# Optimization experiments

Hardware: AMD Instinct MI355X
Metric: run time of the kernel (lower is better)

Reference implementation:

```python
import jax, jax.numpy as jnp
import numpy as np

B, C, L = 4, 64, 4096
RED = 4          # reduction -> q/k channels = C // RED = 16
N_HASHES = 4
HASH_BUCKETS = min(L // 4, 32)  # = 32, matches torch code
EPS = 1e-5


def _conv1x1(x, W, b):
    # x: [B, Cin, L], W: [Cout, Cin], b: [Cout]
    return jnp.einsum('bcl,oc->bol', x, W) + b[None, :, None]


def setup_inputs() -> dict:
    key = jax.random.key(0)
    ks = jax.random.split(key, 12)
    Cq = C // RED
    x = jax.random.normal(ks[0], (B, C, L), dtype=jnp.float32)
    hash_idx = jax.random.randint(ks[1], (B, N_HASHES, L), 0, HASH_BUCKETS, dtype=jnp.int32)
    sC = 1.0 / np.sqrt(C)
    Wq = jax.random.normal(ks[2], (Cq, C), dtype=jnp.float32) * sC
    bq = jax.random.normal(ks[3], (Cq,), dtype=jnp.float32) * 0.01
    Wk = jax.random.normal(ks[4], (Cq, C), dtype=jnp.float32) * sC
    bk = jax.random.normal(ks[5], (Cq,), dtype=jnp.float32) * 0.01
    Wv = jax.random.normal(ks[6], (C, C), dtype=jnp.float32) * sC
    bv = jax.random.normal(ks[7], (C,), dtype=jnp.float32) * 0.01
    Wo = jax.random.normal(ks[8], (C, C), dtype=jnp.float32) * sC
    bo = jax.random.normal(ks[9], (C,), dtype=jnp.float32) * 0.01
    gamma = jax.random.normal(ks[10], (1,), dtype=jnp.float32)  # nonzero so attn path matters
    bn_w = jnp.ones((C,), dtype=jnp.float32)
    bn_b = jnp.zeros((C,), dtype=jnp.float32)
    return dict(x=x, hash_idx=hash_idx, Wq=Wq, bq=bq, Wk=Wk, bk=bk,
                Wv=Wv, bv=bv, Wo=Wo, bo=bo, gamma=gamma, bn_w=bn_w, bn_b=bn_b)


def reference(x, hash_idx, Wq, bq, Wk, bk, Wv, bv, Wo, bo, gamma, bn_w, bn_b):
    # 1x1 conv projections
    q = _conv1x1(x, Wq, bq)   # [B, C/RED, L]
    k = _conv1x1(x, Wk, bk)   # [B, C/RED, L]
    v = _conv1x1(x, Wv, bv)   # [B, C, L]

    qT = q.transpose(0, 2, 1)  # [B, L, Cq]
    kT = k.transpose(0, 2, 1)
    vT = v.transpose(0, 2, 1)  # [B, L, C]

    # raw scores are hash-independent; only the bucket mask changes per hash
    scores = jnp.einsum('bic,bjc->bij', qT, kT)  # [B, L, L], no sqrt(d) scaling (matches torch)

    n_hashes = hash_idx.shape[1]
    acc = jnp.zeros_like(vT)
    for h in range(n_hashes):  # small fixed loop
        idx = hash_idx[:, h, :]                       # [B, L]
        mask = idx[:, :, None] == idx[:, None, :]     # same-bucket mask [B, L, L]
        s = jnp.where(mask, scores, -1e9)
        attn = jax.nn.softmax(s, axis=-1)             # within-bucket softmax (diag always valid)
        acc = acc + jnp.einsum('bij,bjc->bic', attn, vT)
    attn_out = (acc / n_hashes).transpose(0, 2, 1)    # [B, C, L], averaged over hashes

    out = _conv1x1(attn_out, Wo, bo)
    out = gamma * out + x                             # residual with learned scalar

    # BatchNorm1d, training mode: biased batch stats over (B, L) per channel
    mean = out.mean(axis=(0, 2), keepdims=True)
    var = out.var(axis=(0, 2), keepdims=True)
    out = (out - mean) * jax.lax.rsqrt(var + EPS)
    out = out * bn_w[None, :, None] + bn_b[None, :, None]
    return out
```

## Files before the change

kernel.cpp:

```cpp
#include <hip/hip_runtime.h>
#include <math.h>

#define Bn 4
#define Cn 64
#define Ln 4096
#define CQ 16
#define NH 4
#define NB 32
#define EPSV 1e-5f

#define MAXS 384
#define CH2 64
#define KSTR 20
#define VSTR 64

#define QSZ   (Bn*Ln*CQ)
#define VSZ   (Bn*Ln*Cn)
#define ACCSZ (Bn*Ln*Cn)
#define NBH   (Bn*NH)

#define OFF_K   QSZ
#define OFF_V   (2*QSZ)
#define OFF_ACC (2*QSZ + VSZ)

#define LOG2E 1.44269504088896f

__global__ __launch_bounds__(256) void proj_kernel(
        const float* __restrict__ x,
        const float* __restrict__ Wq, const float* __restrict__ bq,
        const float* __restrict__ Wk, const float* __restrict__ bk,
        const float* __restrict__ Wv, const float* __restrict__ bv,
        float* __restrict__ q, float* __restrict__ k, float* __restrict__ v) {
    __shared__ float sWt[Cn*32];
    __shared__ float sb[32];
    int tid = threadIdx.x;
    int third = blockIdx.x % 3;
    int pg    = blockIdx.x / 3;
    int rbase = third * 32;
    for (int idx = tid; idx < Cn*32; idx += 256) {
        int rr = idx & 31, c = idx >> 5;
        int r = rbase + rr;
        float w;
        if (r < 16)      w = Wq[r*Cn + c];
        else if (r < 32) w = Wk[(r-16)*Cn + c];
        else             w = Wv[(r-32)*Cn + c];
        sWt[c*32 + rr] = w;
    }
    if (tid < 32) {
        int r = rbase + tid;
        sb[tid] = (r < 16) ? bq[r] : (r < 32 ? bk[r-16] : bv[r-32]);
    }
    __syncthreads();
    int p = tid & 63, og = tid >> 6;
    int gp = pg * 64 + p;
    int b = gp >> 12, l = gp & (Ln - 1);
    const float* xp = &x[b*Cn*Ln + l];
    int rr0 = og * 8;
    float val[8];
    #pragma unroll
    for (int i = 0; i < 8; i++) val[i] = sb[rr0 + i];
    #pragma unroll
    for (int c0 = 0; c0 < Cn; c0 += 8) {
        float xv[8];
        #pragma unroll
        for (int i = 0; i < 8; i++) xv[i] = xp[(c0 + i)*Ln];
        #pragma unroll
        for (int i = 0; i < 8; i++) {
            const float* wrow = &sWt[(c0 + i)*32 + rr0];
            #pragma unroll
            for (int j = 0; j < 8; j++) val[j] = fmaf(wrow[j], xv[i], val[j]);
        }
    }
    int f = third*8 + og*2;
    float4 t0 = make_float4(val[0], val[1], val[2], val[3]);
    float4 t1 = make_float4(val[4], val[5], val[6], val[7]);
    float4* q4 = (float4*)&q[gp*CQ];
    float4* k4 = (float4*)&k[gp*CQ];
    float4* v4 = (float4*)&v[gp*Cn];
    if (f < 4)      { q4[f]   = t0; q4[f+1] = t1; }
    else if (f < 8) { k4[f-4] = t0; k4[f-3] = t1; }
    else            { v4[f-8] = t0; v4[f-7] = t1; }
}

template<int NS, int MODE>
__device__ __forceinline__ void attn_pass(
        int qbase, int S, int b, int h, int tid,
        const int* list, float* ks, float* vs,
        const float* __restrict__ q, const float* __restrict__ k,
        const float* __restrict__ v, float* __restrict__ acc) {
    int qd = tid >> 2, c4 = tid & 3;
    float4 qr[NS][4];
    float4 o[NS][4];
    float lsum[NS];
    int qi[NS], iqr[NS];
    #pragma unroll
    for (int s = 0; s < NS; s++) {
        qi[s] = qbase + 128*s + qd;
        iqr[s] = 0;
        lsum[s] = 0.f;
        #pragma unroll
        for (int i = 0; i < 4; i++) o[s][i] = make_float4(0.f,0.f,0.f,0.f);
        if (qi[s] < S) {
            iqr[s] = list[qi[s]];
            const float4* qp = (const float4*)&q[(b*Ln + iqr[s])*CQ];
            #pragma unroll
            for (int i = 0; i < 4; i++) {
                float4 t = qp[i];
                t.x*=LOG2E; t.y*=LOG2E; t.z*=LOG2E; t.w*=LOG2E;
                qr[s][i] = t;
            }
        } else {
            #pragma unroll
            for (int i = 0; i < 4; i++) qr[s][i] = make_float4(0.f,0.f,0.f,0.f);
        }
    }
    for (int cc = 0; cc < S; cc += CH2) {
        int nk = min(CH2, S - cc);
        __syncthreads();
        {
            int jj = tid >> 2, cf = tid & 3;
            if (jj < nk) {
                const float4* kp = (const float4*)&k[(b*Ln + list[cc+jj])*CQ];
                *(float4*)&ks[jj*KSTR + cf*4] = kp[cf];
            }
        }
        #pragma unroll
        for (int uu = 0; uu < 2; uu++) {
            int idx = uu*512 + tid;
            int jj = idx >> 4, cf = idx & 15;
            if (jj < nk) {
                const float4* vp = (const float4*)&v[(b*Ln + list[cc+jj])*Cn];
                *(float4*)&vs[jj*VSTR + cf*4] = vp[cf];
            }
        }
        __syncthreads();
        for (int j = 0; j < nk; j++) {
            const float4* kr = (const float4*)&ks[j*KSTR];
            float4 k0 = kr[0], k1 = kr[1], k2 = kr[2], k3 = kr[3];
            const float4* vp4 = (const float4*)&vs[j*VSTR + c4*16];
            float4 v0 = vp4[0], v1 = vp4[1], v2 = vp4[2], v3 = vp4[3];
            #pragma unroll
            for (int s = 0; s < NS; s++) {
                float s0 = qr[s][0].x*k0.x + qr[s][0].y*k0.y + qr[s][0].z*k0.z + qr[s][0].w*k0.w;
                float s1 = qr[s][1].x*k1.x + qr[s][1].y*k1.y + qr[s][1].z*k1.z + qr[s][1].w*k1.w;
                float s2 = qr[s][2].x*k2.x + qr[s][2].y*k2.y + qr[s][2].z*k2.z + qr[s][2].w*k2.w;
                float s3 = qr[s][3].x*k3.x + qr[s][3].y*k3.y + qr[s][3].z*k3.z + qr[s][3].w*k3.w;
                float pw = __builtin_amdgcn_exp2f((s0 + s1) + (s2 + s3));
                lsum[s] += pw;
                o[s][0].x = fmaf(pw, v0.x, o[s][0].x); o[s][0].y = fmaf(pw, v0.y, o[s][0].y);
                o[s][0].z = fmaf(pw, v0.z, o[s][0].z); o[s][0].w = fmaf(pw, v0.w, o[s][0].w);
                o[s][1].x = fmaf(pw, v1.x, o[s][1].x); o[s][1].y = fmaf(pw, v1.y, o[s][1].y);
                o[s][1].z = fmaf(pw, v1.z, o[s][1].z); o[s][1].w = fmaf(pw, v1.w, o[s][1].w);
                o[s][2].x = fmaf(pw, v2.x, o[s][2].x); o[s][2].y = fmaf(pw, v2.y, o[s][2].y);
                o[s][2].z = fmaf(pw, v2.z, o[s][2].z); o[s][2].w = fmaf(pw, v2.w, o[s][2].w);
                o[s][3].x = fmaf(pw, v3.x, o[s][3].x); o[s][3].y = fmaf(pw, v3.y, o[s][3].y);
                o[s][3].z = fmaf(pw, v3.z, o[s][3].z); o[s][3].w = fmaf(pw, v3.w, o[s][3].w);
            }
        }
    }
    #pragma unroll
    for (int s = 0; s < NS; s++) {
        if (qi[s] < S) {
            float inv = 1.f / lsum[s];
            #pragma unroll
            for (int i = 0; i < 4; i++) {
                o[s][i].x*=inv; o[s][i].y*=inv; o[s][i].z*=inv; o[s][i].w*=inv;
            }
            if (MODE == 1) {
                float4* ap = (float4*)&acc[((size_t)h*Bn*Ln + b*Ln + iqr[s])*Cn + c4*16];
                ap[0]=o[s][0]; ap[1]=o[s][1]; ap[2]=o[s][2]; ap[3]=o[s][3];
            } else {
                float* ap = &acc[(b*Ln + iqr[s])*Cn + c4*16];
                #pragma unroll
                for (int i = 0; i < 4; i++) {
                    atomicAdd(&ap[4*i+0], (&o[s][i].x)[0]);
                    atomicAdd(&ap[4*i+1], (&o[s][i].x)[1]);
                    atomicAdd(&ap[4*i+2], (&o[s][i].x)[2]);
                    atomicAdd(&ap[4*i+3], (&o[s][i].x)[3]);
                }
            }
        }
    }
}

template<int MODE>
__global__ __launch_bounds__(512, 4) void attn_kernel(
        const float* __restrict__ q, const float* __restrict__ k,
        const float* __restrict__ v, const int* __restrict__ hidx,
        float* __restrict__ acc) {
    __shared__ int list[MAXS];
    __shared__ float ks[CH2*KSTR];
    __shared__ float vs[CH2*VSTR];
    __shared__ int wtot[8];
    int blk = blockIdx.x;
    int u  = blk & (NB-1);
    int bh = blk >> 5;
    int b  = bh >> 2;
    int h  = bh & 3;
    int tid = threadIdx.x;

    const int4* hp4 = (const int4*)(&hidx[bh*Ln] + tid*8);
    int hv[8];
    {
        int4 t0 = hp4[0], t1 = hp4[1];
        hv[0]=t0.x; hv[1]=t0.y; hv[2]=t0.z; hv[3]=t0.w;
        hv[4]=t1.x; hv[5]=t1.y; hv[6]=t1.z; hv[7]=t1.w;
    }
    int myCnt = 0;
    #pragma unroll
    for (int t = 0; t < 8; t++) myCnt += (hv[t] == u);
    int lane = tid & 63, wv = tid >> 6;
    int pre = myCnt;
    #pragma unroll
    for (int d = 1; d < 64; d <<= 1) {
        int t = __shfl_up(pre, d, 64);
        if (lane >= d) pre += t;
    }
    if (lane == 63) wtot[wv] = pre;
    __syncthreads();
    int base = 0, Sall = 0;
    #pragma unroll
    for (int w = 0; w < 8; w++) {
        base += (w < wv) ? wtot[w] : 0;
        Sall += wtot[w];
    }
    int S = min(Sall, MAXS);
    int excl = base + pre - myCnt;
    #pragma unroll
    for (int t = 0; t < 8; t++) {
        if (hv[t] == u) {
            if (excl < MAXS) list[excl] = tid*8 + t;
            excl++;
        }
    }
    __syncthreads();

    int wq0 = wv * 16;
    for (int qbase = 0; qbase < S; qbase += 256) {
        int rem = S - qbase - wq0;
        if (rem > 128) attn_pass<2,MODE>(qbase,S,b,h,tid,list,ks,vs,q,k,v,acc);
        else           attn_pass<1,MODE>(qbase,S,b,h,tid,list,ks,vs,q,k,v,acc);
    }
}

template<int MODE>
__global__ __launch_bounds__(256) void outconv_kernel(
        const float* __restrict__ acc, const float* __restrict__ Wo,
        const float* __restrict__ bo, const float* __restrict__ gamma,
        const float* __restrict__ x, float* __restrict__ y) {
    __shared__ float sWt[Cn*32];
    __shared__ float sb[32];
    int tid = threadIdx.x;
    int half = blockIdx.x & 1;
    int pg   = blockIdx.x >> 1;
    for (int idx = tid; idx < Cn*32; idx += 256) {
        int oo = idx & 31, c = idx >> 5;
        sWt[c*32 + oo] = Wo[(half*32 + oo)*Cn + c];
    }
    if (tid < 32) sb[tid] = bo[half*32 + tid];
    __syncthreads();
    float g = gamma[0];
    int p = tid & 63, og = tid >> 6;
    int gp = pg * 64 + p;
    int b = gp >> 12, l = gp & (Ln - 1);
    int oo0 = og * 8;
    float val[8];
    #pragma unroll
    for (int i = 0; i < 8; i++) val[i] = sb[oo0 + i];
    const float4* ap0 = (const float4*)&acc[(size_t)gp*Cn];
    #pragma unroll
    for (int c4 = 0; c4 < 16; c4++) {
        float4 t = ap0[c4];
        if (MODE == 1) {
            float4 t1 = ap0[(size_t)ACCSZ/4   + c4];
            float4 t2 = ap0[(size_t)ACCSZ/4*2 + c4];
            float4 t3 = ap0[(size_t)ACCSZ/4*3 + c4];
            t.x += t1.x + t2.x + t3.x; t.y += t1.y + t2.y + t3.y;
            t.z += t1.z + t2.z + t3.z; t.w += t1.w + t2.w + t3.w;
        }
        float a0 = t.x*0.25f, a1 = t.y*0.25f, a2 = t.z*0.25f, a3 = t.w*0.25f;
        const float* w0 = &sWt[(c4*4+0)*32 + oo0];
        const float* w1 = &sWt[(c4*4+1)*32 + oo0];
        const float* w2 = &sWt[(c4*4+2)*32 + oo0];
        const float* w3 = &sWt[(c4*4+3)*32 + oo0];
        #pragma unroll
        for (int i = 0; i < 8; i++) {
            val[i] = fmaf(w0[i], a0, val[i]);
            val[i] = fmaf(w1[i], a1, val[i]);
            val[i] = fmaf(w2[i], a2, val[i]);
            val[i] = fmaf(w3[i], a3, val[i]);
        }
    }
    #pragma unroll
    for (int i = 0; i < 8; i++) {
        int o = half*32 + oo0 + i;
        float yv = fmaf(g, val[i], x[(b*Cn + o)*Ln + l]);
        y[(b*Cn + o)*Ln + l] = yv;
    }
}

__global__ __launch_bounds__(256) void stats_kernel(
        const float* __restrict__ y, float* __restrict__ ssum, float* __restrict__ ssq) {
    int c = blockIdx.x >> 2;
    int part = blockIdx.x & 3;
    int tid = threadIdx.x;
    const float4* yp = (const float4*)&y[(part*Cn + c)*Ln];
    float s = 0.f, s2 = 0.f;
    #pragma unroll
    for (int i = 0; i < 4; i++) {
        float4 t = yp[i*256 + tid];
        s  += t.x + t.y + t.z + t.w;
        s2 += t.x*t.x + t.y*t.y + t.z*t.z + t.w*t.w;
    }
    #pragma unroll
    for (int w = 1; w < 64; w <<= 1) {
        s  += __shfl_xor(s,  w, 64);
        s2 += __shfl_xor(s2, w, 64);
    }
    __shared__ float rs[4], rs2[4];
    int wv = tid >> 6;
    if ((tid & 63) == 0) { rs[wv] = s; rs2[wv] = s2; }
    __syncthreads();
    if (tid == 0) {
        atomicAdd(&ssum[c], rs[0]+rs[1]+rs[2]+rs[3]);
        atomicAdd(&ssq[c],  rs2[0]+rs2[1]+rs2[2]+rs2[3]);
    }
}

__global__ __launch_bounds__(256) void norm_kernel(
        const float* __restrict__ y,
        const float* __restrict__ ssum, const float* __restrict__ ssq,
        const float* __restrict__ bnw, const float* __restrict__ bnb,
        float* __restrict__ out) {
    int idx = blockIdx.x * 256 + threadIdx.x;
    int flat = idx * 4;
    int c = (flat / Ln) & 63;
    const float n = (float)(Bn*Ln);
    float mu = ssum[c] / n;
    float var = ssq[c] / n - mu*mu;
    float is = rsqrtf(var + EPSV);
    float w = is * bnw[c];
    float bb = bnb[c] - mu * w;
    float4 t = ((const float4*)y)[idx];
    float4 r;
    r.x = t.x*w + bb; r.y = t.y*w + bb; r.z = t.z*w + bb; r.w = t.w*w + bb;
    ((float4*)out)[idx] = r;
}

extern "C" void kernel_launch(void* const* d_in, const int* in_sizes, int n_in,
                              void* d_out, int out_size, void* d_ws, size_t ws_size,
                              hipStream_t stream) {
    const float* x    = (const float*)d_in[0];
    const int*   hidx = (const int*)  d_in[1];
    const float* Wq   = (const float*)d_in[2];
    const float* bq   = (const float*)d_in[3];
    const float* Wk   = (const float*)d_in[4];
    const float* bk   = (const float*)d_in[5];
    const float* Wv   = (const float*)d_in[6];
    const float* bv   = (const float*)d_in[7];
    const float* Wo   = (const float*)d_in[8];
    const float* bo   = (const float*)d_in[9];
    const float* gam  = (const float*)d_in[10];
    const float* bnw  = (const float*)d_in[11];
    const float* bnb  = (const float*)d_in[12];
    float* out = (float*)d_out;

    float* ws  = (float*)d_ws;
    float* q   = ws;
    float* k   = ws + OFF_K;
    float* v   = ws + OFF_V;
    float* acc = ws + OFF_ACC;
    float* y   = ws;

    const size_t bigNeed = ((size_t)OFF_ACC + 4*(size_t)ACCSZ + 2*Cn) * sizeof(float);
    bool big = ws_size >= bigNeed;
    float* ssum = acc + (big ? 4*(size_t)ACCSZ : (size_t)ACCSZ);
    float* ssq  = ssum + Cn;

    hipMemsetAsync(ssum, 0, 2*Cn*sizeof(float), stream);

    proj_kernel<<<Bn*Ln/64*3, 256, 0, stream>>>(x, Wq, bq, Wk, bk, Wv, bv, q, k, v);
    if (big) {
        attn_kernel<1><<<NBH*NB, 512, 0, stream>>>(q, k, v, hidx, acc);
        outconv_kernel<1><<<Bn*Ln/64*2, 256, 0, stream>>>(acc, Wo, bo, gam, x, y);
    } else {
        hipMemsetAsync(acc, 0, (size_t)ACCSZ*sizeof(float), stream);
        attn_kernel<0><<<NBH*NB, 512, 0, stream>>>(q, k, v, hidx, acc);
        outconv_kernel<0><<<Bn*Ln/64*2, 256, 0, stream>>>(acc, Wo, bo, gam, x, y);
    }
    stats_kernel<<<Cn*4, 256, 0, stream>>>(y, ssum, ssq);
    norm_kernel<<<Bn*Cn*Ln/4/256, 256, 0, stream>>>(y, ssum, ssq, bnw, bnb, out);
}
```

Measured before the change: 187.2 us.

## Split attention key loop across two block halves and drop stats memset

The attention block now splits its 8 waves into two halves that each process half of a 128-key chunk for the same 64-query tile. The partial outputs and softmax sums are merged through shared memory before normalization. The goal is to halve the query tile per pass so that small buckets keep more waves busy and the loop has less serial length per thread. In exchange it adds extra barriers, a shared-memory reduction step and a larger K/V staging tile. Separately, the BN stats kernel writes per-block partial sums that the norm kernel adds up, which removes the memset and the atomics.

Result: slower. 200.2 us (+7.0%).

```diff
diff --git a/kernel.cpp b/kernel.cpp
--- a/kernel.cpp
+++ b/kernel.cpp
@@ -10,7 +10,7 @@
 #define EPSV 1e-5f
 
 #define MAXS 384
-#define CH2 64
+#define CH2 128
 #define KSTR 20
 #define VSTR 64
 
@@ -84,25 +84,27 @@
 
 template<int NS, int MODE>
 __device__ __forceinline__ void attn_pass(
-        int qbase, int S, int b, int h, int tid,
-        const int* list, float* ks, float* vs,
+        int qbase, int S, int b, int h, int half, int rem, int tid,
+        const int* list, float* ks, float* vs, float* lsm,
         const float* __restrict__ q, const float* __restrict__ k,
         const float* __restrict__ v, float* __restrict__ acc) {
-    int qd = tid >> 2, c4 = tid & 3;
+    int qd = (tid >> 2) & 63;
+    int c4 = tid & 3;
+    int mx = tid & 255;
     float4 qr[NS][4];
     float4 o[NS][4];
     float lsum[NS];
     int qi[NS], iqr[NS];
     #pragma unroll
     for (int s = 0; s < NS; s++) {
-        qi[s] = qbase + 128*s + qd;
+        qi[s] = qbase + 64*s + qd;
         iqr[s] = 0;
         lsum[s] = 0.f;
         #pragma unroll
         for (int i = 0; i < 4; i++) o[s][i] = make_float4(0.f,0.f,0.f,0.f);
         if (qi[s] < S) {
             iqr[s] = list[qi[s]];
-            const float4* qp = (const float4*)&q[(b*Ln + iqr[s])*CQ];
+            const float4* qp = (const float4*)&q[((size_t)b*Ln + iqr[s])*CQ];
             #pragma unroll
             for (int i = 0; i < 4; i++) {
                 float4 t = qp[i];
@@ -120,63 +122,87 @@
         {
             int jj = tid >> 2, cf = tid & 3;
             if (jj < nk) {
-                const float4* kp = (const float4*)&k[(b*Ln + list[cc+jj])*CQ];
+                const float4* kp = (const float4*)&k[((size_t)b*Ln + list[cc+jj])*CQ];
                 *(float4*)&ks[jj*KSTR + cf*4] = kp[cf];
             }
         }
         #pragma unroll
-        for (int uu = 0; uu < 2; uu++) {
+        for (int uu = 0; uu < 4; uu++) {
             int idx = uu*512 + tid;
             int jj = idx >> 4, cf = idx & 15;
             if (jj < nk) {
-                const float4* vp = (const float4*)&v[(b*Ln + list[cc+jj])*Cn];
+                const float4* vp = (const float4*)&v[((size_t)b*Ln + list[cc+jj])*Cn];
                 *(float4*)&vs[jj*VSTR + cf*4] = vp[cf];
             }
         }
         __syncthreads();
-        for (int j = 0; j < nk; j++) {
-            const float4* kr = (const float4*)&ks[j*KSTR];
-            float4 k0 = kr[0], k1 = kr[1], k2 = kr[2], k3 = kr[3];
-            const float4* vp4 = (const float4*)&vs[j*VSTR + c4*16];
-            float4 v0 = vp4[0], v1 = vp4[1], v2 = vp4[2], v3 = vp4[3];
-            #pragma unroll
-            for (int s = 0; s < NS; s++) {
-                float s0 = qr[s][0].x*k0.x + qr[s][0].y*k0.y + qr[s][0].z*k0.z + qr[s][0].w*k0.w;
-                float s1 = qr[s][1].x*k1.x + qr[s][1].y*k1.y + qr[s][1].z*k1.z + qr[s][1].w*k1.w;
-                float s2 = qr[s][2].x*k2.x + qr[s][2].y*k2.y + qr[s][2].z*k2.z + qr[s][2].w*k2.w;
-                float s3 = qr[s][3].x*k3.x + qr[s][3].y*k3.y + qr[s][3].z*k3.z + qr[s][3].w*k3.w;
-                float pw = __builtin_amdgcn_exp2f((s0 + s1) + (s2 + s3));
-                lsum[s] += pw;
-                o[s][0].x = fmaf(pw, v0.x, o[s][0].x); o[s][0].y = fmaf(pw, v0.y, o[s][0].y);
-                o[s][0].z = fmaf(pw, v0.z, o[s][0].z); o[s][0].w = fmaf(pw, v0.w, o[s][0].w);
-                o[s][1].x = fmaf(pw, v1.x, o[s][1].x); o[s][1].y = fmaf(pw, v1.y, o[s][1].y);
-                o[s][1].z = fmaf(pw, v1.z, o[s][1].z); o[s][1].w = fmaf(pw, v1.w, o[s][1].w);
-                o[s][2].x = fmaf(pw, v2.x, o[s][2].x); o[s][2].y = fmaf(pw, v2.y, o[s][2].y);
-                o[s][2].z = fmaf(pw, v2.z, o[s][2].z); o[s][2].w = fmaf(pw, v2.w, o[s][2].w);
-                o[s][3].x = fmaf(pw, v3.x, o[s][3].x); o[s][3].y = fmaf(pw, v3.y, o[s][3].y);
-                o[s][3].z = fmaf(pw, v3.z, o[s][3].z); o[s][3].w = fmaf(pw, v3.w, o[s][3].w);
+        if (rem > 0) {
+            int jh1 = min(nk, half*64 + 64);
+            for (int j = half*64; j < jh1; j++) {
+                const float4* kr = (const float4*)&ks[j*KSTR];
+                float4 k0 = kr[0], k1 = kr[1], k2 = kr[2], k3 = kr[3];
+                const float4* vp4 = (const float4*)&vs[j*VSTR + c4*16];
+                float4 v0 = vp4[0], v1 = vp4[1], v2 = vp4[2], v3 = vp4[3];
+                #pragma unroll
+                for (int s = 0; s < NS; s++) {
+                    float s0 = qr[s][0].x*k0.x + qr[s][0].y*k0.y + qr[s][0].z*k0.z + qr[s][0].w*k0.w;
+                    float s1 = qr[s][1].x*k1.x + qr[s][1].y*k1.y + qr[s][1].z*k1.z + qr[s][1].w*k1.w;
+                    float s2 = qr[s][2].x*k2.x + qr[s][2].y*k2.y + qr[s][2].z*k2.z + qr[s][2].w*k2.w;
+                    float s3 = qr[s][3].x*k3.x + qr[s][3].y*k3.y + qr[s][3].z*k3.z + qr[s][3].w*k3.w;
+                    float pw = __builtin_amdgcn_exp2f((s0 + s1) + (s2 + s3));
+                    lsum[s] += pw;
+                    o[s][0].x = fmaf(pw, v0.x, o[s][0].x); o[s][0].y = fmaf(pw, v0.y, o[s][0].y);
+                    o[s][0].z = fmaf(pw, v0.z, o[s][0].z); o[s][0].w = fmaf(pw, v0.w, o[s][0].w);
+                    o[s][1].x = fmaf(pw, v1.x, o[s][1].x); o[s][1].y = fmaf(pw, v1.y, o[s][1].y);
+                    o[s][1].z = fmaf(pw, v1.z, o[s][1].z); o[s][1].w = fmaf(pw, v1.w, o[s][1].w);
+                    o[s][2].x = fmaf(pw, v2.x, o[s][2].x); o[s][2].y = fmaf(pw, v2.y, o[s][2].y);
+                    o[s][2].z = fmaf(pw, v2.z, o[s][2].z); o[s][2].w = fmaf(pw, v2.w, o[s][2].w);
+                    o[s][3].x = fmaf(pw, v3.x, o[s][3].x); o[s][3].y = fmaf(pw, v3.y, o[s][3].y);
+                    o[s][3].z = fmaf(pw, v3.z, o[s][3].z); o[s][3].w = fmaf(pw, v3.w, o[s][3].w);
+                }
             }
         }
     }
     #pragma unroll
-    for (int s = 0; s < NS; s++) {
-        if (qi[s] < S) {
-            float inv = 1.f / lsum[s];
-            #pragma unroll
-            for (int i = 0; i < 4; i++) {
-                o[s][i].x*=inv; o[s][i].y*=inv; o[s][i].z*=inv; o[s][i].w*=inv;
-            }
-            if (MODE == 1) {
-                float4* ap = (float4*)&acc[((size_t)h*Bn*Ln + b*Ln + iqr[s])*Cn + c4*16];
-                ap[0]=o[s][0]; ap[1]=o[s][1]; ap[2]=o[s][2]; ap[3]=o[s][3];
-            } else {
-                float* ap = &acc[(b*Ln + iqr[s])*Cn + c4*16];
+    for (int s = 0; s < 2; s++) {
+        __syncthreads();
+        if (s < NS && half == 1 && qi[s] < S) {
+            float4* wb = (float4*)&vs[mx*16];
+            wb[0]=o[s][0]; wb[1]=o[s][1]; wb[2]=o[s][2]; wb[3]=o[s][3];
+            if (c4 == 0) lsm[qd] = lsum[s];
+        }
+        __syncthreads();
+        if (s < NS && half == 0 && qi[s] < S) {
+            const float4* rb = (const float4*)&vs[mx*16];
+            float4 p0 = rb[0], p1 = rb[1], p2 = rb[2], p3 = rb[3];
+            o[s][0].x+=p0.x; o[s][0].y+=p0.y; o[s][0].z+=p0.z; o[s][0].w+=p0.w;
+            o[s][1].x+=p1.x; o[s][1].y+=p1.y; o[s][1].z+=p1.z; o[s][1].w+=p1.w;
+            o[s][2].x+=p2.x; o[s][2].y+=p2.y; o[s][2].z+=p2.z; o[s][2].w+=p2.w;
+            o[s][3].x+=p3.x; o[s][3].y+=p3.y; o[s][3].z+=p3.z; o[s][3].w+=p3.w;
+            lsum[s] += lsm[qd];
+        }
+    }
+    if (half == 0) {
+        #pragma unroll
+        for (int s = 0; s < NS; s++) {
+            if (qi[s] < S) {
+                float inv = 1.f / lsum[s];
                 #pragma unroll
                 for (int i = 0; i < 4; i++) {
-                    atomicAdd(&ap[4*i+0], (&o[s][i].x)[0]);
-                    atomicAdd(&ap[4*i+1], (&o[s][i].x)[1]);
-                    atomicAdd(&ap[4*i+2], (&o[s][i].x)[2]);
-                    atomicAdd(&ap[4*i+3], (&o[s][i].x)[3]);
+                    o[s][i].x*=inv; o[s][i].y*=inv; o[s][i].z*=inv; o[s][i].w*=inv;
+                }
+                if (MODE == 1) {
+                    float4* ap = (float4*)&acc[((size_t)h*Bn*Ln + b*Ln + iqr[s])*Cn + c4*16];
+                    ap[0]=o[s][0]; ap[1]=o[s][1]; ap[2]=o[s][2]; ap[3]=o[s][3];
+                } else {
+                    float* ap = &acc[((size_t)b*Ln + iqr[s])*Cn + c4*16];
+                    #pragma unroll
+                    for (int i = 0; i < 4; i++) {
+                        atomicAdd(&ap[4*i+0], (&o[s][i].x)[0]);
+                        atomicAdd(&ap[4*i+1], (&o[s][i].x)[1]);
+                        atomicAdd(&ap[4*i+2], (&o[s][i].x)[2]);
+                        atomicAdd(&ap[4*i+3], (&o[s][i].x)[3]);
+                    }
                 }
             }
         }
@@ -191,6 +217,7 @@
     __shared__ int list[MAXS];
     __shared__ float ks[CH2*KSTR];
     __shared__ float vs[CH2*VSTR];
+    __shared__ float lsm[64];
     __shared__ int wtot[8];
     int blk = blockIdx.x;
     int u  = blk & (NB-1);
@@ -235,11 +262,12 @@
     }
     __syncthreads();
 
-    int wq0 = wv * 16;
-    for (int qbase = 0; qbase < S; qbase += 256) {
+    int half = wv >> 2;
+    int wq0 = (wv & 3) * 16;
+    for (int qbase = 0; qbase < S; qbase += 128) {
         int rem = S - qbase - wq0;
-        if (rem > 128) attn_pass<2,MODE>(qbase,S,b,h,tid,list,ks,vs,q,k,v,acc);
-        else           attn_pass<1,MODE>(qbase,S,b,h,tid,list,ks,vs,q,k,v,acc);
+        if (rem > 64) attn_pass<2,MODE>(qbase,S,b,h,half,rem,tid,list,ks,vs,lsm,q,k,v,acc);
+        else          attn_pass<1,MODE>(qbase,S,b,h,half,rem,tid,list,ks,vs,lsm,q,k,v,acc);
     }
 }
 
@@ -300,7 +328,7 @@
 }
 
 __global__ __launch_bounds__(256) void stats_kernel(
-        const float* __restrict__ y, float* __restrict__ ssum, float* __restrict__ ssq) {
+        const float* __restrict__ y, float* __restrict__ ssumP, float* __restrict__ ssqP) {
     int c = blockIdx.x >> 2;
     int part = blockIdx.x & 3;
     int tid = threadIdx.x;
@@ -322,22 +350,25 @@
     if ((tid & 63) == 0) { rs[wv] = s; rs2[wv] = s2; }
     __syncthreads();
     if (tid == 0) {
-        atomicAdd(&ssum[c], rs[0]+rs[1]+rs[2]+rs[3]);
-        atomicAdd(&ssq[c],  rs2[0]+rs2[1]+rs2[2]+rs2[3]);
+        ssumP[blockIdx.x] = rs[0]+rs[1]+rs[2]+rs[3];
+        ssqP[blockIdx.x]  = rs2[0]+rs2[1]+rs2[2]+rs2[3];
     }
 }
 
 __global__ __launch_bounds__(256) void norm_kernel(
         const float* __restrict__ y,
-        const float* __restrict__ ssum, const float* __restrict__ ssq,
+        const float* __restrict__ ssumP, const float* __restrict__ ssqP,
         const float* __restrict__ bnw, const float* __restrict__ bnb,
         float* __restrict__ out) {
     int idx = blockIdx.x * 256 + threadIdx.x;
     int flat = idx * 4;
     int c = (flat / Ln) & 63;
+    float s = 0.f, s2 = 0.f;
+    #pragma unroll
+    for (int hh = 0; hh < 4; hh++) { s += ssumP[c*4+hh]; s2 += ssqP[c*4+hh]; }
     const float n = (float)(Bn*Ln);
-    float mu = ssum[c] / n;
-    float var = ssq[c] / n - mu*mu;
+    float mu = s / n;
+    float var = s2 / n - mu*mu;
     float is = rsqrtf(var + EPSV);
     float w = is * bnw[c];
     float bb = bnb[c] - mu * w;
@@ -372,12 +403,10 @@
     float* acc = ws + OFF_ACC;
     float* y   = ws;
 
-    const size_t bigNeed = ((size_t)OFF_ACC + 4*(size_t)ACCSZ + 2*Cn) * sizeof(float);
+    const size_t bigNeed = ((size_t)OFF_ACC + 4*(size_t)ACCSZ + 512) * sizeof(float);
     bool big = ws_size >= bigNeed;
-    float* ssum = acc + (big ? 4*(size_t)ACCSZ : (size_t)ACCSZ);
-    float* ssq  = ssum + Cn;
-
-    hipMemsetAsync(ssum, 0, 2*Cn*sizeof(float), stream);
+    float* ssumP = acc + (big ? 4*(size_t)ACCSZ : (size_t)ACCSZ);
+    float* ssqP  = ssumP + 256;
 
     proj_kernel<<<Bn*Ln/64*3, 256, 0, stream>>>(x, Wq, bq, Wk, bk, Wv, bv, q, k, v);
     if (big) {
@@ -388,6 +417,6 @@
         attn_kernel<0><<<NBH*NB, 512, 0, stream>>>(q, k, v, hidx, acc);
         outconv_kernel<0><<<Bn*Ln/64*2, 256, 0, stream>>>(acc, Wo, bo, gam, x, y);
     }
-    stats_kernel<<<Cn*4, 256, 0, stream>>>(y, ssum, ssq);
-    norm_kernel<<<Bn*Cn*Ln/4/256, 256, 0, stream>>>(y, ssum, ssq, bnw, bnb, out);
-}
+    stats_kernel<<<Cn*4, 256, 0, stream>>>(y, ssumP, ssqP);
+    norm_kernel<<<Bn*Cn*Ln/4/256, 256, 0, stream>>>(y, ssumP, ssqP, bnw, bnb, out);
+}
```
